# Kernel tuning notes

Measured on AMD Instinct MI355X. Metric: run time of the kernel, lower is better.

Reference implementation:

```python
import jax, jax.numpy as jnp
import numpy as np

# dims: n=batch, T=n_shifts, dX=16, dU=8, H=256 hidden, L=128 ldim, K=64 n_aux (L=2K)

def setup_inputs() -> dict:
    key = jax.random.key(0)
    ks = jax.random.split(key, 16)
    n, T, dX, dU, H, L, K = 64, 64, 16, 8, 256, 128, 64
    def lin(k, fan_in, shape):
        return (jax.random.uniform(k, shape, jnp.float32) * 2.0 - 1.0) / np.sqrt(fan_in)
    xs = jax.random.normal(ks[0], (n, T, dX), jnp.float32)
    us = jax.random.normal(ks[1], (n, T - 1, dU), jnp.float32)
    theta = jax.random.uniform(ks[2], (K,), jnp.float32) * (2.0 * np.pi)
    inp = {
        'xs': xs, 'us': us,
        # stacked x-aux encoders (K copies): BN affine, 3 linear layers (last no bias), output scale
        'x_gamma': jnp.ones((K, dX)), 'x_beta': jnp.zeros((K, dX)),
        'xW1': lin(ks[3], dX, (K, dX, H)), 'xb1': jnp.zeros((K, H)),
        'xW2': lin(ks[4], H, (K, H, H)), 'xb2': jnp.zeros((K, H)),
        'xW3': lin(ks[5], H, (K, H, L)), 'x_scale': jnp.ones((K, L)),
        # stacked u-aux encoders (K copies)
        'u_gamma': jnp.ones((K, dU)), 'u_beta': jnp.zeros((K, dU)),
        'uW1': lin(ks[6], dU, (K, dU, H)), 'ub1': jnp.zeros((K, H)),
        'uW2': lin(ks[7], H, (K, H, H)), 'ub2': jnp.zeros((K, H)),
        'uW3': lin(ks[8], H, (K, H, L)), 'u_scale': jnp.ones((K, L)),
        # Jordan-block complex eigenvalues (|lam| ~ 0.95)
        'reL': 0.95 * jnp.cos(theta), 'imL': 0.95 * jnp.sin(theta),
        # decoder C: Linear(ldim, dim, bias=False) -> weight [dX, L]
        'C_W': lin(ks[9], L, (dX, L)),
    }
    return inp


def _encoder(x, gamma, beta, W1, b1, W2, b2, W3, scale):
    # x: [M, D]; stacked params over K nets. BN stats (training mode) are per-feature over M,
    # identical across nets since the same x feeds every net.
    mu = x.mean(0)
    var = ((x - mu) ** 2).mean(0)
    xn = (x - mu) * jax.lax.rsqrt(var + 1e-5)          # [M, D]
    h = xn[None] * gamma[:, None, :] + beta[:, None, :]  # [K, M, D]
    h = jax.nn.leaky_relu(jnp.einsum('kmd,kdh->kmh', h, W1) + b1[:, None, :])
    h = jax.nn.leaky_relu(jnp.einsum('kmd,kdh->kmh', h, W2) + b2[:, None, :])
    h = jnp.einsum('kmd,kdh->kmh', h, W3)               # last layer: no bias
    return h * scale[:, None, :]                        # [K, M, L]


def reference(xs, us, x_gamma, x_beta, xW1, xb1, xW2, xb2, xW3, x_scale,
              u_gamma, u_beta, uW1, ub1, uW2, ub2, uW3, u_scale, reL, imL, C_W):
    n, T, dX = xs.shape
    K = reL.shape[0]
    L = 2 * K
    Tm1 = T - 1
    # phi1s: [n, T, K(net), K(pair), 2]
    phi = _encoder(xs.reshape(n * T, dX), x_gamma, x_beta, xW1, xb1, xW2, xb2, xW3, x_scale)
    phi1s = jnp.moveaxis(phi, 0, 1).reshape(n, T, K, K, 2)
    # ures = psi(u) - psi(0): [n, T-1, K, K, 2]
    uflat = us.reshape(n * Tm1, -1)
    psi_u = _encoder(uflat, u_gamma, u_beta, uW1, ub1, uW2, ub2, uW3, u_scale)
    psi_0 = _encoder(jnp.zeros_like(uflat), u_gamma, u_beta, uW1, ub1, uW2, ub2, uW3, u_scale)
    ures = jnp.moveaxis(psi_u - psi_0, 0, 1).reshape(n, Tm1, K, K, 2)
    # block-diagonal Koopman: per net j a 2x2 rotation-scale [[re, im], [-im, re]]
    R = jnp.stack([jnp.stack([reL, imL], -1), jnp.stack([-imL, reL], -1)], -2)  # [K, 2, 2]

    def step(p, u_t):
        p = jnp.einsum('bjkc,jcd->bjkd', p + u_t, R)
        return p, p

    _, preds = jax.lax.scan(step, phi1s[:, 0], jnp.moveaxis(ures, 0, 1))
    preds = jnp.moveaxis(preds, 0, 1)  # [n, T-1, K, K, 2]

    def phi2y(p):
        # sum over net axis (-3), flatten pair dims -> [.., L], decode with C
        return p.sum(-3).reshape(*p.shape[:-3], L) @ C_W.T

    y = phi2y(phi1s[:, 1:])
    y_pred = phi2y(preds)
    return y, y_pred
```

## Files before the change

kernel.cpp:

```cpp
#include <hip/hip_runtime.h>

typedef __bf16 bf16_t;
typedef __bf16 bf16x8 __attribute__((ext_vector_type(8)));
typedef __bf16 bf16x4 __attribute__((ext_vector_type(4)));
typedef float  f32x4  __attribute__((ext_vector_type(4)));

__global__ __launch_bounds__(256) void prep_all_kernel(
    const float* __restrict__ xW1, const float* __restrict__ xb1,
    const float* __restrict__ xg,  const float* __restrict__ xbeta,
    const float* __restrict__ uW1, const float* __restrict__ ub1,
    const float* __restrict__ ug,  const float* __restrict__ ubeta,
    const float* __restrict__ xW2, const float* __restrict__ uW2,
    const float* __restrict__ xW3, const float* __restrict__ uW3,
    const float* __restrict__ x_scale, const float* __restrict__ u_scale,
    const float* __restrict__ ub2,
    const float* __restrict__ xs, const float* __restrict__ us,
    bf16_t* __restrict__ xW1t, float* __restrict__ xb1p,
    bf16_t* __restrict__ uW1t, float* __restrict__ ub1p,
    bf16_t* __restrict__ xW2t, bf16_t* __restrict__ uW2t,
    bf16_t* __restrict__ xW3t, bf16_t* __restrict__ uW3t,
    float* __restrict__ psi0, float* __restrict__ part)
{
    const int t = blockIdx.x, tid = threadIdx.x;
    __shared__ float tile[32][33];
    __shared__ float h1[256], h2[256];

    if (t < 12288) {
        const float* in; bf16_t* outp; const float* scale = nullptr;
        int j, r0, c0, C;
        if (t < 8192) {
            C = 256;
            j = (t & 4095) >> 6;
            const int tl = t & 63; r0 = (tl >> 3) * 32; c0 = (tl & 7) * 32;
            if (t < 4096) { in = xW2; outp = xW2t; }
            else          { in = uW2; outp = uW2t; }
        } else {
            C = 128;
            const int l = t - 8192;
            j = (l & 2047) >> 5;
            const int tl = l & 31; r0 = (tl >> 2) * 32; c0 = (tl & 3) * 32;
            if (l < 2048) { in = xW3; outp = xW3t; scale = x_scale + j * 128; }
            else          { in = uW3; outp = uW3t; scale = u_scale + j * 128; }
        }
        const int R = 256;
        in   += (size_t)j * R * C;
        bf16_t* op = outp + (size_t)j * R * C;
        const int tx = tid & 31, ty = tid >> 5;
        #pragma unroll
        for (int i = 0; i < 4; i++)
            tile[ty + i * 8][tx] = in[(size_t)(r0 + ty + i * 8) * C + c0 + tx];
        __syncthreads();
        #pragma unroll
        for (int i = 0; i < 4; i++) {
            int c = c0 + ty + i * 8;
            float sc = scale ? scale[c] : 1.f;
            op[(size_t)c * R + r0 + tx] = (bf16_t)(tile[tx][ty + i * 8] * sc);
        }
    } else if (t < 12416) {
        const int bid = t - 12288, j = bid & 63, h = tid;
        const float *W1, *b1, *gamma, *beta; bf16_t* W1t; float* b1p; int D;
        if (bid < 64) { W1 = xW1; b1 = xb1; gamma = xg; beta = xbeta; W1t = xW1t; b1p = xb1p; D = 16; }
        else          { W1 = uW1; b1 = ub1; gamma = ug; beta = ubeta; W1t = uW1t; b1p = ub1p; D = 8; }
        float bacc = b1[j * 256 + h];
        bf16_t* orow = W1t + (size_t)(j * 256 + h) * 32;
        for (int d = 0; d < 32; d++) orow[d] = (bf16_t)0.f;
        for (int d = 0; d < D; d++) {
            float w = W1[((size_t)j * D + d) * 256 + h];
            orow[d] = (bf16_t)(gamma[j * D + d] * w);
            bacc += beta[j * D + d] * w;
        }
        b1p[j * 256 + h] = bacc;
    } else if (t < 12480) {
        const int j = t - 12416, h = tid;
        {
            float bacc = ub1[j * 256 + h];
            #pragma unroll
            for (int d = 0; d < 8; d++)
                bacc += ubeta[j * 8 + d] * uW1[((size_t)j * 8 + d) * 256 + h];
            h1[h] = fmaxf(bacc, 0.01f * bacc);
        }
        __syncthreads();
        {
            float acc = ub2[j * 256 + h];
            const float* w2 = uW2 + (size_t)j * 65536 + h;
            #pragma unroll 8
            for (int d = 0; d < 256; d++) acc += h1[d] * w2[d * 256];
            h2[h] = fmaxf(acc, 0.01f * acc);
        }
        __syncthreads();
        if (h < 128) {
            float acc = 0.f;
            const float* w3 = uW3 + (size_t)j * 32768 + h;
            #pragma unroll 8
            for (int d = 0; d < 256; d++) acc += h2[d] * w3[d * 128];
            psi0[j * 128 + h] = acc * u_scale[j * 128 + h];
        }
    } else {
        const int bid = t - 12480;
        const bool isx = bid < 64;
        const float* x = isx ? xs : us;
        const int D   = isx ? 16 : 8;
        const int lb  = isx ? bid : bid - 64;
        const int per = isx ? 1024 : 1008;
        const int start = lb * per;
        float a = 0.f, b = 0.f;
        for (int idx = start + tid; idx < start + per; idx += 256) {
            float v = x[idx];
            a += v; b += v * v;
        }
        float* s1 = h1; float* s2 = h2;
        s1[tid] = a; s2[tid] = b;
        __syncthreads();
        if (tid < D) {
            float sa = 0.f, sb = 0.f;
            for (int k = tid; k < 256; k += D) { sa += s1[k]; sb += s2[k]; }
            part[bid * 32 + tid]      = sa;
            part[bid * 32 + 16 + tid] = sb;
        }
    }
}

__global__ __launch_bounds__(512, 4) void fused_mlp_kernel(
    const float* __restrict__ xs, const float* __restrict__ us,
    const float* __restrict__ part,
    const bf16_t* __restrict__ xW1t, const float* __restrict__ xb1p,
    const bf16_t* __restrict__ xW2t, const float* __restrict__ xb2,
    const bf16_t* __restrict__ xW3t,
    const bf16_t* __restrict__ uW1t, const float* __restrict__ ub1p,
    const bf16_t* __restrict__ uW2t, const float* __restrict__ ub2,
    const bf16_t* __restrict__ uW3t,
    bf16_t* __restrict__ phi, bf16_t* __restrict__ psiu)
{
    const int bid  = blockIdx.x;
    const int xcd  = bid & 7;
    const int slot = bid >> 3;
    const int band = slot >> 6;
    const int t64  = slot & 63;
    const int j    = xcd * 8 + band;
    const bool is_x = t64 < 32;
    const int tile  = is_x ? t64 : (t64 - 32);

    const float*  In  = is_x ? xs   : us;
    const int     D   = is_x ? 16   : 8;
    const bf16_t* W1t = is_x ? xW1t : uW1t;
    const float*  b1p = is_x ? xb1p : ub1p;
    const bf16_t* W2t = is_x ? xW2t : uW2t;
    const float*  b2  = is_x ? xb2  : ub2;
    const bf16_t* W3t = is_x ? xW3t : uW3t;
    bf16_t* outp      = is_x ? phi  : psiu;
    const int M       = is_x ? 4096 : 4032;

    const int row0 = tile * 128;
    const int tid  = threadIdx.x;
    const int wave = tid >> 6;
    const int lane = tid & 63;
    const int quad = lane >> 4;
    const int l16  = lane & 15;
    const int lo2  = l16 & 3, hi2 = l16 >> 2;

    __shared__ __align__(16) bf16_t hs[128 * 256];
    __shared__ float stats_s[32];

    if (tid < 16) {
        if (is_x) {
            float sa = 0.f, sb = 0.f;
            #pragma unroll 8
            for (int b = 0; b < 64; b++) { sa += part[b * 32 + tid]; sb += part[b * 32 + 16 + tid]; }
            float mu = sa / 4096.f, var = sb / 4096.f - mu * mu;
            stats_s[tid] = mu; stats_s[16 + tid] = rsqrtf(var + 1e-5f);
        } else if (tid < 8) {
            float sa = 0.f, sb = 0.f;
            #pragma unroll 8
            for (int b = 64; b < 96; b++) { sa += part[b * 32 + tid]; sb += part[b * 32 + 16 + tid]; }
            float mu = sa / 4032.f, var = sb / 4032.f - mu * mu;
            stats_s[tid] = mu; stats_s[16 + tid] = rsqrtf(var + 1e-5f);
        }
    }
    __syncthreads();

    const f32x4 vzero = {0.f, 0.f, 0.f, 0.f};

    char* const hsB = (char*)hs;
    const char* const abase = hsB + l16 * 512 + ((quad ^ lo2) << 4);
    const int  wlow0 = (quad >> 1) ^ lo2;
    char* const wbase = hsB + l16 * 512 + ((wave ^ hi2) << 6) + ((quad & 1) << 3);

    {
        bf16x8 wfr[2];
        #pragma unroll
        for (int nbi = 0; nbi < 2; nbi++)
            wfr[nbi] = *reinterpret_cast<const bf16x8*>(
                W1t + (size_t)(j * 256 + wave * 32 + nbi * 16 + l16) * 32 + quad * 8);

        f32x4 acc[8][2];
        #pragma unroll
        for (int a = 0; a < 8; a++) { acc[a][0] = vzero; acc[a][1] = vzero; }

        const int c0 = quad * 8;
        #pragma unroll
        for (int mb = 0; mb < 8; mb++) {
            bf16x8 a;
            if (c0 < D) {
                int row = row0 + mb * 16 + l16;
                if (row > M - 1) row = M - 1;
                const float* xp = In + (size_t)row * D + c0;
                f32x4 v0 = *reinterpret_cast<const f32x4*>(xp);
                f32x4 v1 = *reinterpret_cast<const f32x4*>(xp + 4);
                #pragma unroll
                for (int e = 0; e < 4; e++) a[e]     = (bf16_t)((v0[e] - stats_s[c0 + e])     * stats_s[16 + c0 + e]);
                #pragma unroll
                for (int e = 0; e < 4; e++) a[4 + e] = (bf16_t)((v1[e] - stats_s[c0 + 4 + e]) * stats_s[16 + c0 + 4 + e]);
            } else {
                #pragma unroll
                for (int e = 0; e < 8; e++) a[e] = (bf16_t)0.f;
            }
            #pragma unroll
            for (int nbi = 0; nbi < 2; nbi++)
                acc[mb][nbi] = __builtin_amdgcn_mfma_f32_16x16x32_bf16(
                    wfr[nbi], a, acc[mb][nbi], 0, 0, 0);
        }

        #pragma unroll
        for (int nbi = 0; nbi < 2; nbi++) {
            const f32x4 bias = *reinterpret_cast<const f32x4*>(
                b1p + j * 256 + wave * 32 + nbi * 16 + quad * 4);
            char* wp = wbase + ((wlow0 ^ (nbi << 1)) << 4);
            #pragma unroll
            for (int mb = 0; mb < 8; mb++) {
                bf16x4 pk;
                #pragma unroll
                for (int r = 0; r < 4; r++) {
                    float v = acc[mb][nbi][r] + bias[r];
                    v = fmaxf(v, 0.01f * v);
                    pk[r] = (bf16_t)v;
                }
                *reinterpret_cast<bf16x4*>(wp + mb * 8192) = pk;
            }
        }
    }
    __syncthreads();

    {
        f32x4 acc[8][2];
        #pragma unroll
        for (int a = 0; a < 8; a++) { acc[a][0] = vzero; acc[a][1] = vzero; }

        const bf16_t* w2base = W2t + ((size_t)j * 256 + wave * 32 + l16) * 256 + quad * 8;

        bf16x8 wr[3][2];
        #pragma unroll
        for (int d = 0; d < 3; d++)
            #pragma unroll
            for (int nbi = 0; nbi < 2; nbi++)
                wr[d][nbi] = *reinterpret_cast<const bf16x8*>(w2base + nbi * 4096 + d * 32);

        #pragma unroll
        for (int kk = 0; kk < 8; kk++) {
            const int c = kk % 3;
            const char* ap = abase + ((kk ^ hi2) << 6);
            bf16x8 av0[4];
            #pragma unroll
            for (int mb = 0; mb < 4; mb++)
                av0[mb] = *reinterpret_cast<const bf16x8*>(ap + mb * 8192);
            #pragma unroll
            for (int nbi = 0; nbi < 2; nbi++)
                #pragma unroll
                for (int mb = 0; mb < 4; mb++)
                    acc[mb][nbi] = __builtin_amdgcn_mfma_f32_16x16x32_bf16(
                        wr[c][nbi], av0[mb], acc[mb][nbi], 0, 0, 0);
            bf16x8 av1[4];
            #pragma unroll
            for (int mb = 0; mb < 4; mb++)
                av1[mb] = *reinterpret_cast<const bf16x8*>(ap + (mb + 4) * 8192);
            #pragma unroll
            for (int nbi = 0; nbi < 2; nbi++)
                #pragma unroll
                for (int mb = 4; mb < 8; mb++)
                    acc[mb][nbi] = __builtin_amdgcn_mfma_f32_16x16x32_bf16(
                        wr[c][nbi], av1[mb - 4], acc[mb][nbi], 0, 0, 0);
            if (kk < 5) {
                #pragma unroll
                for (int nbi = 0; nbi < 2; nbi++)
                    wr[c][nbi] = *reinterpret_cast<const bf16x8*>(
                        w2base + nbi * 4096 + (kk + 3) * 32);
            }
        }
        __syncthreads();
        #pragma unroll
        for (int nbi = 0; nbi < 2; nbi++) {
            const f32x4 bias = *reinterpret_cast<const f32x4*>(
                b2 + j * 256 + wave * 32 + nbi * 16 + quad * 4);
            char* wp = wbase + ((wlow0 ^ (nbi << 1)) << 4);
            #pragma unroll
            for (int mb = 0; mb < 8; mb++) {
                bf16x4 pk;
                #pragma unroll
                for (int r = 0; r < 4; r++) {
                    float v = acc[mb][nbi][r] + bias[r];
                    v = fmaxf(v, 0.01f * v);
                    pk[r] = (bf16_t)v;
                }
                *reinterpret_cast<bf16x4*>(wp + mb * 8192) = pk;
            }
        }
    }
    __syncthreads();

    {
        f32x4 acc[8];
        #pragma unroll
        for (int a = 0; a < 8; a++) acc[a] = vzero;

        const bf16_t* w3base = W3t + ((size_t)j * 128 + wave * 16 + l16) * 256 + quad * 8;

        bf16x8 wr[3];
        #pragma unroll
        for (int d = 0; d < 3; d++)
            wr[d] = *reinterpret_cast<const bf16x8*>(w3base + d * 32);

        #pragma unroll
        for (int kk = 0; kk < 8; kk++) {
            const int c = kk % 3;
            const char* ap = abase + ((kk ^ hi2) << 6);
            bf16x8 av0[4];
            #pragma unroll
            for (int mb = 0; mb < 4; mb++)
                av0[mb] = *reinterpret_cast<const bf16x8*>(ap + mb * 8192);
            #pragma unroll
            for (int mb = 0; mb < 4; mb++)
                acc[mb] = __builtin_amdgcn_mfma_f32_16x16x32_bf16(
                    wr[c], av0[mb], acc[mb], 0, 0, 0);
            bf16x8 av1[4];
            #pragma unroll
            for (int mb = 0; mb < 4; mb++)
                av1[mb] = *reinterpret_cast<const bf16x8*>(ap + (mb + 4) * 8192);
            #pragma unroll
            for (int mb = 4; mb < 8; mb++)
                acc[mb] = __builtin_amdgcn_mfma_f32_16x16x32_bf16(
                    wr[c], av1[mb - 4], acc[mb], 0, 0, 0);
            if (kk < 5)
                wr[c] = *reinterpret_cast<const bf16x8*>(w3base + (kk + 3) * 32);
        }
        __syncthreads();
        {
            const int sp3 = (wave * 2 + (quad >> 1)) ^ l16;
            char* w3p = hsB + l16 * 256 + sp3 * 16 + ((quad & 1) << 3);
            #pragma unroll
            for (int mb = 0; mb < 8; mb++) {
                bf16x4 pk;
                #pragma unroll
                for (int r = 0; r < 4; r++) pk[r] = (bf16_t)acc[mb][r];
                *reinterpret_cast<bf16x4*>(w3p + mb * 4096) = pk;
            }
        }
    }
    __syncthreads();
    #pragma unroll
    for (int p = 0; p < 4; p++) {
        const int rr = p * 32 + (tid >> 4);
        const int s  = tid & 15;
        if (row0 + rr < M) {
            bf16x8 v = *reinterpret_cast<const bf16x8*>(hs + rr * 128 + (s ^ (rr & 15)) * 8);
            *reinterpret_cast<bf16x8*>(outp + ((size_t)j * M + row0 + rr) * 128 + s * 8) = v;
        }
    }
}

__global__ __launch_bounds__(256) void y_kernel(
    const bf16_t* __restrict__ phi, const float* __restrict__ C_W,
    float* __restrict__ y) {
    const int m0 = blockIdx.x * 16;
    const int tid = threadIdx.x;
    __shared__ float S[16][128];
    __shared__ float Cs[2048];
    #pragma unroll
    for (int i = 0; i < 8; i++) Cs[tid + i * 256] = C_W[tid + i * 256];
    const int r  = tid >> 4;
    const int cg = (tid & 15) * 8;
    float acc[8];
    #pragma unroll
    for (int e = 0; e < 8; e++) acc[e] = 0.f;
    const bf16_t* p = phi + (size_t)(m0 + r) * 128 + cg;
    for (int j = 0; j < 64; j++) {
        bf16x8 v = *reinterpret_cast<const bf16x8*>(p + (size_t)j * 524288);
        #pragma unroll
        for (int e = 0; e < 8; e++) acc[e] += (float)v[e];
    }
    #pragma unroll
    for (int e = 0; e < 8; e++) S[r][cg + e] = acc[e];
    __syncthreads();
    const int mm = tid >> 4, o = tid & 15;
    const int m = m0 + mm;
    if ((m & 63) != 0) {
        float a = 0.f;
        #pragma unroll 8
        for (int l = 0; l < 128; l++) a += S[mm][l] * Cs[o * 128 + l];
        const int b = m >> 6, ti = (m & 63) - 1;
        y[(b * 63 + ti) * 16 + o] = a;
    }
}

__global__ __launch_bounds__(256) void scan_kernel(
    const bf16_t* __restrict__ phi, const bf16_t* __restrict__ psiu,
    const float* __restrict__ psi0, const float* __restrict__ reL,
    const float* __restrict__ imL, float* __restrict__ scratch) {
    const int b = blockIdx.x >> 3, jg = blockIdx.x & 7;
    const int tid = threadIdx.x;
    const int wave = tid >> 6, lane = tid & 63;
    __shared__ float red[2][4][128];

    const int j0 = jg * 8 + wave * 2;
    float sx0, sy0, sx1, sy1;
    float p0x0, p0y0, p0x1, p0y1, lre0, lim0, lre1, lim1;
    {
        unsigned v0 = *reinterpret_cast<const unsigned*>(
            phi + ((size_t)j0 * 4096 + b * 64) * 128 + lane * 2);
        unsigned v1 = *reinterpret_cast<const unsigned*>(
            phi + ((size_t)(j0 + 1) * 4096 + b * 64) * 128 + lane * 2);
        sx0 = __uint_as_float(v0 << 16); sy0 = __uint_as_float(v0 & 0xFFFF0000u);
        sx1 = __uint_as_float(v1 << 16); sy1 = __uint_as_float(v1 & 0xFFFF0000u);
        float2 p0 = *reinterpret_cast<const float2*>(psi0 + j0 * 128 + lane * 2);
        float2 p1 = *reinterpret_cast<const float2*>(psi0 + (j0 + 1) * 128 + lane * 2);
        p0x0 = p0.x; p0y0 = p0.y; p0x1 = p1.x; p0y1 = p1.y;
        lre0 = reL[j0]; lim0 = imL[j0]; lre1 = reL[j0 + 1]; lim1 = imL[j0 + 1];
    }
    const bf16_t* up0 = psiu + ((size_t)j0 * 4032 + b * 63) * 128 + lane * 2;
    const bf16_t* up1 = psiu + ((size_t)(j0 + 1) * 4032 + b * 63) * 128 + lane * 2;
    unsigned cur0 = *reinterpret_cast<const unsigned*>(up0);
    unsigned cur1 = *reinterpret_cast<const unsigned*>(up1);
    float* out = scratch + (size_t)blockIdx.x * 63 * 128;

    for (int t = 0; t < 63; t++) {
        unsigned nx0 = 0, nx1 = 0;
        if (t < 62) {
            nx0 = *reinterpret_cast<const unsigned*>(up0 + (t + 1) * 128);
            nx1 = *reinterpret_cast<const unsigned*>(up1 + (t + 1) * 128);
        }
        float px = sx0 + (__uint_as_float(cur0 << 16) - p0x0);
        float py = sy0 + (__uint_as_float(cur0 & 0xFFFF0000u) - p0y0);
        sx0 = px * lre0 - py * lim0;
        sy0 = px * lim0 + py * lre0;
        px = sx1 + (__uint_as_float(cur1 << 16) - p0x1);
        py = sy1 + (__uint_as_float(cur1 & 0xFFFF0000u) - p0y1);
        sx1 = px * lre1 - py * lim1;
        sy1 = px * lim1 + py * lre1;
        const int db = t & 1;
        red[db][wave][lane * 2]     = sx0 + sx1;
        red[db][wave][lane * 2 + 1] = sy0 + sy1;
        __syncthreads();
        if (tid < 128)
            out[t * 128 + tid] = red[db][0][tid] + red[db][1][tid]
                               + red[db][2][tid] + red[db][3][tid];
        cur0 = nx0; cur1 = nx1;
    }
}

__global__ __launch_bounds__(64) void decode_kernel(
    const float* __restrict__ scratch, const float* __restrict__ C_W,
    float* __restrict__ ypred) {
    const int t = blockIdx.x, b = blockIdx.y, l = threadIdx.x;
    __shared__ float S[128];
    float s0 = 0.f, s1 = 0.f;
    #pragma unroll
    for (int jg = 0; jg < 8; jg++) {
        float2 v = *reinterpret_cast<const float2*>(
            scratch + ((size_t)(b * 8 + jg) * 63 + t) * 128 + l * 2);
        s0 += v.x; s1 += v.y;
    }
    S[l * 2] = s0; S[l * 2 + 1] = s1;
    __syncthreads();
    const int o = l >> 2, q = l & 3;
    float acc = 0.f;
    #pragma unroll
    for (int i = 0; i < 32; i++)
        acc += S[q * 32 + i] * C_W[o * 128 + q * 32 + i];
    acc += __shfl_xor(acc, 2, 4);
    acc += __shfl_xor(acc, 1, 4);
    if (q == 0) ypred[(b * 63 + t) * 16 + o] = acc;
}

extern "C" void kernel_launch(void* const* d_in, const int* in_sizes, int n_in,
                              void* d_out, int out_size, void* d_ws, size_t ws_size,
                              hipStream_t stream) {
    const float* xs      = (const float*)d_in[0];
    const float* us      = (const float*)d_in[1];
    const float* x_gamma = (const float*)d_in[2];
    const float* x_beta  = (const float*)d_in[3];
    const float* xW1     = (const float*)d_in[4];
    const float* xb1     = (const float*)d_in[5];
    const float* xW2     = (const float*)d_in[6];
    const float* xb2     = (const float*)d_in[7];
    const float* xW3     = (const float*)d_in[8];
    const float* x_scale = (const float*)d_in[9];
    const float* u_gamma = (const float*)d_in[10];
    const float* u_beta  = (const float*)d_in[11];
    const float* uW1     = (const float*)d_in[12];
    const float* ub1     = (const float*)d_in[13];
    const float* uW2     = (const float*)d_in[14];
    const float* ub2     = (const float*)d_in[15];
    const float* uW3     = (const float*)d_in[16];
    const float* u_scale = (const float*)d_in[17];
    const float* reL     = (const float*)d_in[18];
    const float* imL     = (const float*)d_in[19];
    const float* C_W     = (const float*)d_in[20];

    char* ws = (char*)d_ws;
    size_t off = 0;
    auto alloc = [&](size_t bytes) -> char* {
        char* p = ws + off;
        off += (bytes + 255) & ~(size_t)255;
        return p;
    };
    float*  part = (float*)alloc(96 * 32 * 4);
    bf16_t* xW1t = (bf16_t*)alloc((size_t)64 * 256 * 32 * 2);
    float*  xb1p = (float*) alloc((size_t)64 * 256 * 4);
    bf16_t* xW2t = (bf16_t*)alloc((size_t)64 * 256 * 256 * 2);
    bf16_t* xW3t = (bf16_t*)alloc((size_t)64 * 128 * 256 * 2);
    bf16_t* uW1t = (bf16_t*)alloc((size_t)64 * 256 * 32 * 2);
    float*  ub1p = (float*) alloc((size_t)64 * 256 * 4);
    bf16_t* uW2t = (bf16_t*)alloc((size_t)64 * 256 * 256 * 2);
    bf16_t* uW3t = (bf16_t*)alloc((size_t)64 * 128 * 256 * 2);
    float*  psi0 = (float*) alloc((size_t)64 * 128 * 4);
    bf16_t* phi  = (bf16_t*)alloc((size_t)64 * 4096 * 128 * 2);
    bf16_t* psiu = (bf16_t*)alloc((size_t)64 * 4032 * 128 * 2);
    float*  scr  = (float*) alloc((size_t)512 * 63 * 128 * 4);

    float* y_out     = (float*)d_out;
    float* ypred_out = y_out + 64 * 63 * 16;

    prep_all_kernel<<<12576, 256, 0, stream>>>(
        xW1, xb1, x_gamma, x_beta, uW1, ub1, u_gamma, u_beta,
        xW2, uW2, xW3, uW3, x_scale, u_scale, ub2, xs, us,
        xW1t, xb1p, uW1t, ub1p, xW2t, uW2t, xW3t, uW3t, psi0, part);
    fused_mlp_kernel<<<4096, 512, 0, stream>>>(
        xs, us, part,
        xW1t, xb1p, xW2t, xb2, xW3t, uW1t, ub1p, uW2t, ub2, uW3t, phi, psiu);
    y_kernel<<<256, 256, 0, stream>>>(phi, C_W, y_out);
    scan_kernel<<<512, 256, 0, stream>>>(phi, psiu, psi0, reL, imL, scr);
    decode_kernel<<<dim3(63, 64), 64, 0, stream>>>(scr, C_W, ypred_out);
}
```

Before: 362.7 us.

## Retile fused MLP waves to 64x64 output blocks and merge y and scan kernels

The fused MLP now splits its 8 waves into a 2x4 grid, so each wave computes a 64-row by 64-column tile instead of all 128 rows by 32 columns. This halves the LDS activation reads per MFMA and reuses each A fragment across four weight fragments. The shared-memory write swizzle and the layer-2 weight prefetch (now double-buffered) are rewritten to match. Separately, the y-decode and scan kernels are merged into one launch, with block index choosing the role, to save a kernel launch and let both run concurrently.

```diff
diff --git a/kernel.cpp b/kernel.cpp
--- a/kernel.cpp
+++ b/kernel.cpp
@@ -158,6 +158,12 @@
     const int l16  = lane & 15;
     const int lo2  = l16 & 3, hi2 = l16 >> 2;
 
+    const int nw = wave & 3;
+    const int mw = wave >> 2;
+    const int m0 = mw * 64;
+    const int n0 = nw * 64;
+    const int n3 = (wave & 3) * 32;
+
     __shared__ __align__(16) bf16_t hs[128 * 256];
     __shared__ float stats_s[32];
 
@@ -181,27 +187,27 @@
     const f32x4 vzero = {0.f, 0.f, 0.f, 0.f};
 
     char* const hsB = (char*)hs;
-    const char* const abase = hsB + l16 * 512 + ((quad ^ lo2) << 4);
-    const int  wlow0 = (quad >> 1) ^ lo2;
-    char* const wbase = hsB + l16 * 512 + ((wave ^ hi2) << 6) + ((quad & 1) << 3);
+    const char* const abase = hsB + (m0 + l16) * 512 + ((quad ^ lo2) << 4);
 
     {
-        bf16x8 wfr[2];
-        #pragma unroll
-        for (int nbi = 0; nbi < 2; nbi++)
+        bf16x8 wfr[4];
+        #pragma unroll
+        for (int nbi = 0; nbi < 4; nbi++)
             wfr[nbi] = *reinterpret_cast<const bf16x8*>(
-                W1t + (size_t)(j * 256 + wave * 32 + nbi * 16 + l16) * 32 + quad * 8);
-
-        f32x4 acc[8][2];
-        #pragma unroll
-        for (int a = 0; a < 8; a++) { acc[a][0] = vzero; acc[a][1] = vzero; }
+                W1t + (size_t)(j * 256 + n0 + nbi * 16 + l16) * 32 + quad * 8);
+
+        f32x4 acc[4][4];
+        #pragma unroll
+        for (int a = 0; a < 4; a++)
+            #pragma unroll
+            for (int c = 0; c < 4; c++) acc[a][c] = vzero;
 
         const int c0 = quad * 8;
         #pragma unroll
-        for (int mb = 0; mb < 8; mb++) {
+        for (int mb = 0; mb < 4; mb++) {
             bf16x8 a;
             if (c0 < D) {
-                int row = row0 + mb * 16 + l16;
+                int row = row0 + m0 + mb * 16 + l16;
                 if (row > M - 1) row = M - 1;
                 const float* xp = In + (size_t)row * D + c0;
                 f32x4 v0 = *reinterpret_cast<const f32x4*>(xp);
@@ -215,18 +221,19 @@
                 for (int e = 0; e < 8; e++) a[e] = (bf16_t)0.f;
             }
             #pragma unroll
-            for (int nbi = 0; nbi < 2; nbi++)
+            for (int nbi = 0; nbi < 4; nbi++)
                 acc[mb][nbi] = __builtin_amdgcn_mfma_f32_16x16x32_bf16(
                     wfr[nbi], a, acc[mb][nbi], 0, 0, 0);
         }
 
         #pragma unroll
-        for (int nbi = 0; nbi < 2; nbi++) {
+        for (int nbi = 0; nbi < 4; nbi++) {
             const f32x4 bias = *reinterpret_cast<const f32x4*>(
-                b1p + j * 256 + wave * 32 + nbi * 16 + quad * 4);
-            char* wp = wbase + ((wlow0 ^ (nbi << 1)) << 4);
-            #pragma unroll
-            for (int mb = 0; mb < 8; mb++) {
+                b1p + j * 256 + n0 + nbi * 16 + quad * 4);
+            const int g = (n0 >> 3) + nbi * 2 + (quad >> 1);
+            char* wrow = hsB + (m0 + l16) * 512 + ((g ^ l16) << 4) + ((quad & 1) << 3);
+            #pragma unroll
+            for (int mb = 0; mb < 4; mb++) {
                 bf16x4 pk;
                 #pragma unroll
                 for (int r = 0; r < 4; r++) {
@@ -234,65 +241,56 @@
                     v = fmaxf(v, 0.01f * v);
                     pk[r] = (bf16_t)v;
                 }
-                *reinterpret_cast<bf16x4*>(wp + mb * 8192) = pk;
+                *reinterpret_cast<bf16x4*>(wrow + mb * 8192) = pk;
             }
         }
     }
     __syncthreads();
 
     {
-        f32x4 acc[8][2];
-        #pragma unroll
-        for (int a = 0; a < 8; a++) { acc[a][0] = vzero; acc[a][1] = vzero; }
-
-        const bf16_t* w2base = W2t + ((size_t)j * 256 + wave * 32 + l16) * 256 + quad * 8;
-
-        bf16x8 wr[3][2];
-        #pragma unroll
-        for (int d = 0; d < 3; d++)
-            #pragma unroll
-            for (int nbi = 0; nbi < 2; nbi++)
-                wr[d][nbi] = *reinterpret_cast<const bf16x8*>(w2base + nbi * 4096 + d * 32);
+        f32x4 acc[4][4];
+        #pragma unroll
+        for (int a = 0; a < 4; a++)
+            #pragma unroll
+            for (int c = 0; c < 4; c++) acc[a][c] = vzero;
+
+        const bf16_t* w2base = W2t + ((size_t)j * 256 + n0 + l16) * 256 + quad * 8;
+
+        bf16x8 wr[2][4];
+        #pragma unroll
+        for (int nbi = 0; nbi < 4; nbi++)
+            wr[0][nbi] = *reinterpret_cast<const bf16x8*>(w2base + nbi * 4096);
 
         #pragma unroll
         for (int kk = 0; kk < 8; kk++) {
-            const int c = kk % 3;
+            const int cb = kk & 1, nb = cb ^ 1;
+            if (kk < 7) {
+                #pragma unroll
+                for (int nbi = 0; nbi < 4; nbi++)
+                    wr[nb][nbi] = *reinterpret_cast<const bf16x8*>(
+                        w2base + nbi * 4096 + (kk + 1) * 32);
+            }
             const char* ap = abase + ((kk ^ hi2) << 6);
-            bf16x8 av0[4];
+            bf16x8 av[4];
             #pragma unroll
             for (int mb = 0; mb < 4; mb++)
-                av0[mb] = *reinterpret_cast<const bf16x8*>(ap + mb * 8192);
-            #pragma unroll
-            for (int nbi = 0; nbi < 2; nbi++)
+                av[mb] = *reinterpret_cast<const bf16x8*>(ap + mb * 8192);
+            #pragma unroll
+            for (int nbi = 0; nbi < 4; nbi++)
                 #pragma unroll
                 for (int mb = 0; mb < 4; mb++)
                     acc[mb][nbi] = __builtin_amdgcn_mfma_f32_16x16x32_bf16(
-                        wr[c][nbi], av0[mb], acc[mb][nbi], 0, 0, 0);
-            bf16x8 av1[4];
-            #pragma unroll
-            for (int mb = 0; mb < 4; mb++)
-                av1[mb] = *reinterpret_cast<const bf16x8*>(ap + (mb + 4) * 8192);
-            #pragma unroll
-            for (int nbi = 0; nbi < 2; nbi++)
-                #pragma unroll
-                for (int mb = 4; mb < 8; mb++)
-                    acc[mb][nbi] = __builtin_amdgcn_mfma_f32_16x16x32_bf16(
-                        wr[c][nbi], av1[mb - 4], acc[mb][nbi], 0, 0, 0);
-            if (kk < 5) {
-                #pragma unroll
-                for (int nbi = 0; nbi < 2; nbi++)
-                    wr[c][nbi] = *reinterpret_cast<const bf16x8*>(
-                        w2base + nbi * 4096 + (kk + 3) * 32);
-            }
-        }
-        __syncthreads();
-        #pragma unroll
-        for (int nbi = 0; nbi < 2; nbi++) {
+                        wr[cb][nbi], av[mb], acc[mb][nbi], 0, 0, 0);
+        }
+        __syncthreads();
+        #pragma unroll
+        for (int nbi = 0; nbi < 4; nbi++) {
             const f32x4 bias = *reinterpret_cast<const f32x4*>(
-                b2 + j * 256 + wave * 32 + nbi * 16 + quad * 4);
-            char* wp = wbase + ((wlow0 ^ (nbi << 1)) << 4);
-            #pragma unroll
-            for (int mb = 0; mb < 8; mb++) {
+                b2 + j * 256 + n0 + nbi * 16 + quad * 4);
+            const int g = (n0 >> 3) + nbi * 2 + (quad >> 1);
+            char* wrow = hsB + (m0 + l16) * 512 + ((g ^ l16) << 4) + ((quad & 1) << 3);
+            #pragma unroll
+            for (int mb = 0; mb < 4; mb++) {
                 bf16x4 pk;
                 #pragma unroll
                 for (int r = 0; r < 4; r++) {
@@ -300,57 +298,58 @@
                     v = fmaxf(v, 0.01f * v);
                     pk[r] = (bf16_t)v;
                 }
-                *reinterpret_cast<bf16x4*>(wp + mb * 8192) = pk;
+                *reinterpret_cast<bf16x4*>(wrow + mb * 8192) = pk;
             }
         }
     }
     __syncthreads();
 
     {
-        f32x4 acc[8];
-        #pragma unroll
-        for (int a = 0; a < 8; a++) acc[a] = vzero;
-
-        const bf16_t* w3base = W3t + ((size_t)j * 128 + wave * 16 + l16) * 256 + quad * 8;
-
-        bf16x8 wr[3];
+        f32x4 acc[4][2];
+        #pragma unroll
+        for (int a = 0; a < 4; a++) { acc[a][0] = vzero; acc[a][1] = vzero; }
+
+        const bf16_t* w3base = W3t + ((size_t)j * 128 + n3 + l16) * 256 + quad * 8;
+
+        bf16x8 wr[3][2];
         #pragma unroll
         for (int d = 0; d < 3; d++)
-            wr[d] = *reinterpret_cast<const bf16x8*>(w3base + d * 32);
+            #pragma unroll
+            for (int nbi = 0; nbi < 2; nbi++)
+                wr[d][nbi] = *reinterpret_cast<const bf16x8*>(w3base + nbi * 4096 + d * 32);
 
         #pragma unroll
         for (int kk = 0; kk < 8; kk++) {
             const int c = kk % 3;
             const char* ap = abase + ((kk ^ hi2) << 6);
-            bf16x8 av0[4];
+            bf16x8 av[4];
             #pragma unroll
             for (int mb = 0; mb < 4; mb++)
-                av0[mb] = *reinterpret_cast<const bf16x8*>(ap + mb * 8192);
-            #pragma unroll
-            for (int mb = 0; mb < 4; mb++)
-                acc[mb] = __builtin_amdgcn_mfma_f32_16x16x32_bf16(
-                    wr[c], av0[mb], acc[mb], 0, 0, 0);
-            bf16x8 av1[4];
-            #pragma unroll
-            for (int mb = 0; mb < 4; mb++)
-                av1[mb] = *reinterpret_cast<const bf16x8*>(ap + (mb + 4) * 8192);
-            #pragma unroll
-            for (int mb = 4; mb < 8; mb++)
-                acc[mb] = __builtin_amdgcn_mfma_f32_16x16x32_bf16(
-                    wr[c], av1[mb - 4], acc[mb], 0, 0, 0);
-            if (kk < 5)
-                wr[c] = *reinterpret_cast<const bf16x8*>(w3base + (kk + 3) * 32);
-        }
-        __syncthreads();
-        {
-            const int sp3 = (wave * 2 + (quad >> 1)) ^ l16;
-            char* w3p = hsB + l16 * 256 + sp3 * 16 + ((quad & 1) << 3);
-            #pragma unroll
-            for (int mb = 0; mb < 8; mb++) {
+                av[mb] = *reinterpret_cast<const bf16x8*>(ap + mb * 8192);
+            #pragma unroll
+            for (int nbi = 0; nbi < 2; nbi++)
+                #pragma unroll
+                for (int mb = 0; mb < 4; mb++)
+                    acc[mb][nbi] = __builtin_amdgcn_mfma_f32_16x16x32_bf16(
+                        wr[c][nbi], av[mb], acc[mb][nbi], 0, 0, 0);
+            if (kk < 5) {
+                #pragma unroll
+                for (int nbi = 0; nbi < 2; nbi++)
+                    wr[c][nbi] = *reinterpret_cast<const bf16x8*>(
+                        w3base + nbi * 4096 + (kk + 3) * 32);
+            }
+        }
+        __syncthreads();
+        #pragma unroll
+        for (int nbi = 0; nbi < 2; nbi++) {
+            const int g = (n3 >> 3) + nbi * 2 + (quad >> 1);
+            char* wrow = hsB + (m0 + l16) * 256 + ((g ^ l16) << 4) + ((quad & 1) << 3);
+            #pragma unroll
+            for (int mb = 0; mb < 4; mb++) {
                 bf16x4 pk;
                 #pragma unroll
-                for (int r = 0; r < 4; r++) pk[r] = (bf16_t)acc[mb][r];
-                *reinterpret_cast<bf16x4*>(w3p + mb * 4096) = pk;
+                for (int r = 0; r < 4; r++) pk[r] = (bf16_t)acc[mb][nbi][r];
+                *reinterpret_cast<bf16x4*>(wrow + mb * 4096) = pk;
             }
         }
     }
@@ -366,48 +365,48 @@
     }
 }
 
-__global__ __launch_bounds__(256) void y_kernel(
-    const bf16_t* __restrict__ phi, const float* __restrict__ C_W,
-    float* __restrict__ y) {
-    const int m0 = blockIdx.x * 16;
+__global__ __launch_bounds__(256) void scan_y_kernel(
+    const bf16_t* __restrict__ phi, const bf16_t* __restrict__ psiu,
+    const float* __restrict__ psi0, const float* __restrict__ reL,
+    const float* __restrict__ imL, const float* __restrict__ C_W,
+    float* __restrict__ scratch, float* __restrict__ y) {
     const int tid = threadIdx.x;
+    __shared__ float red[2][4][128];
     __shared__ float S[16][128];
     __shared__ float Cs[2048];
-    #pragma unroll
-    for (int i = 0; i < 8; i++) Cs[tid + i * 256] = C_W[tid + i * 256];
-    const int r  = tid >> 4;
-    const int cg = (tid & 15) * 8;
-    float acc[8];
-    #pragma unroll
-    for (int e = 0; e < 8; e++) acc[e] = 0.f;
-    const bf16_t* p = phi + (size_t)(m0 + r) * 128 + cg;
-    for (int j = 0; j < 64; j++) {
-        bf16x8 v = *reinterpret_cast<const bf16x8*>(p + (size_t)j * 524288);
-        #pragma unroll
-        for (int e = 0; e < 8; e++) acc[e] += (float)v[e];
-    }
-    #pragma unroll
-    for (int e = 0; e < 8; e++) S[r][cg + e] = acc[e];
-    __syncthreads();
-    const int mm = tid >> 4, o = tid & 15;
-    const int m = m0 + mm;
-    if ((m & 63) != 0) {
-        float a = 0.f;
-        #pragma unroll 8
-        for (int l = 0; l < 128; l++) a += S[mm][l] * Cs[o * 128 + l];
-        const int b = m >> 6, ti = (m & 63) - 1;
-        y[(b * 63 + ti) * 16 + o] = a;
-    }
-}
-
-__global__ __launch_bounds__(256) void scan_kernel(
-    const bf16_t* __restrict__ phi, const bf16_t* __restrict__ psiu,
-    const float* __restrict__ psi0, const float* __restrict__ reL,
-    const float* __restrict__ imL, float* __restrict__ scratch) {
+
+    if (blockIdx.x >= 512) {
+        const int m0 = (blockIdx.x - 512) * 16;
+        #pragma unroll
+        for (int i = 0; i < 8; i++) Cs[tid + i * 256] = C_W[tid + i * 256];
+        const int r  = tid >> 4;
+        const int cg = (tid & 15) * 8;
+        float acc[8];
+        #pragma unroll
+        for (int e = 0; e < 8; e++) acc[e] = 0.f;
+        const bf16_t* p = phi + (size_t)(m0 + r) * 128 + cg;
+        for (int j = 0; j < 64; j++) {
+            bf16x8 v = *reinterpret_cast<const bf16x8*>(p + (size_t)j * 524288);
+            #pragma unroll
+            for (int e = 0; e < 8; e++) acc[e] += (float)v[e];
+        }
+        #pragma unroll
+        for (int e = 0; e < 8; e++) S[r][cg + e] = acc[e];
+        __syncthreads();
+        const int mm = tid >> 4, o = tid & 15;
+        const int m = m0 + mm;
+        if ((m & 63) != 0) {
+            float a = 0.f;
+            #pragma unroll 8
+            for (int l = 0; l < 128; l++) a += S[mm][l] * Cs[o * 128 + l];
+            const int b = m >> 6, ti = (m & 63) - 1;
+            y[(b * 63 + ti) * 16 + o] = a;
+        }
+        return;
+    }
+
     const int b = blockIdx.x >> 3, jg = blockIdx.x & 7;
-    const int tid = threadIdx.x;
     const int wave = tid >> 6, lane = tid & 63;
-    __shared__ float red[2][4][128];
 
     const int j0 = jg * 8 + wave * 2;
     float sx0, sy0, sx1, sy1;
@@ -535,7 +534,6 @@
     fused_mlp_kernel<<<4096, 512, 0, stream>>>(
         xs, us, part,
         xW1t, xb1p, xW2t, xb2, xW3t, uW1t, ub1p, uW2t, ub2, uW3t, phi, psiu);
-    y_kernel<<<256, 256, 0, stream>>>(phi, C_W, y_out);
-    scan_kernel<<<512, 256, 0, stream>>>(phi, psiu, psi0, reL, imL, scr);
+    scan_y_kernel<<<768, 256, 0, stream>>>(phi, psiu, psi0, reL, imL, C_W, scr, y_out);
     decode_kernel<<<dim3(63, 64), 64, 0, stream>>>(scr, C_W, ypred_out);
 }
```

New measurement: 433.3 us. 1.19x slower.

## Fuse y, scan and decode kernels; enlarge transpose tiles in prep

Applied to the files above, without the earlier changes.

Merges y_kernel, scan_kernel and decode_kernel into one 512-thread kernel. Blocks 0-63 each run the full per-batch scan over all 64 nets and decode y_pred in place, so the fp32 scratch buffer and its round trip go away. Blocks 64 and up compute y with 4-way unrolled loads. The weight-transpose part of prep now uses 64x32 tiles, which halves its block count. The trade-off is less scan parallelism (64 blocks instead of 512) and an extra barrier per timestep, in exchange for two fewer launches and less global traffic.

```diff
diff --git a/kernel.cpp b/kernel.cpp
--- a/kernel.cpp
+++ b/kernel.cpp
@@ -22,42 +22,42 @@
     float* __restrict__ psi0, float* __restrict__ part)
 {
     const int t = blockIdx.x, tid = threadIdx.x;
-    __shared__ float tile[32][33];
+    __shared__ float tile[32][65];
     __shared__ float h1[256], h2[256];
 
-    if (t < 12288) {
+    if (t < 6144) {
         const float* in; bf16_t* outp; const float* scale = nullptr;
         int j, r0, c0, C;
-        if (t < 8192) {
+        if (t < 4096) {
             C = 256;
-            j = (t & 4095) >> 6;
-            const int tl = t & 63; r0 = (tl >> 3) * 32; c0 = (tl & 7) * 32;
-            if (t < 4096) { in = xW2; outp = xW2t; }
+            j = (t & 2047) >> 5;
+            const int tl = t & 31; r0 = (tl >> 3) * 64; c0 = (tl & 7) * 32;
+            if (t < 2048) { in = xW2; outp = xW2t; }
             else          { in = uW2; outp = uW2t; }
         } else {
             C = 128;
-            const int l = t - 8192;
-            j = (l & 2047) >> 5;
-            const int tl = l & 31; r0 = (tl >> 2) * 32; c0 = (tl & 3) * 32;
-            if (l < 2048) { in = xW3; outp = xW3t; scale = x_scale + j * 128; }
+            const int l = t - 4096;
+            j = (l & 1023) >> 4;
+            const int tl = l & 15; r0 = (tl >> 2) * 64; c0 = (tl & 3) * 32;
+            if (l < 1024) { in = xW3; outp = xW3t; scale = x_scale + j * 128; }
             else          { in = uW3; outp = uW3t; scale = u_scale + j * 128; }
         }
-        const int R = 256;
-        in   += (size_t)j * R * C;
-        bf16_t* op = outp + (size_t)j * R * C;
-        const int tx = tid & 31, ty = tid >> 5;
-        #pragma unroll
-        for (int i = 0; i < 4; i++)
-            tile[ty + i * 8][tx] = in[(size_t)(r0 + ty + i * 8) * C + c0 + tx];
-        __syncthreads();
-        #pragma unroll
-        for (int i = 0; i < 4; i++) {
-            int c = c0 + ty + i * 8;
-            float sc = scale ? scale[c] : 1.f;
-            op[(size_t)c * R + r0 + tx] = (bf16_t)(tile[tx][ty + i * 8] * sc);
-        }
-    } else if (t < 12416) {
-        const int bid = t - 12288, j = bid & 63, h = tid;
+        in += (size_t)j * 256 * C;
+        bf16_t* op = outp + (size_t)j * 256 * C;
+        const int cx = tid & 31, ry0 = tid >> 5;
+        #pragma unroll
+        for (int p = 0; p < 8; p++)
+            tile[cx][ry0 + p * 8] = in[(size_t)(r0 + ry0 + p * 8) * C + c0 + cx];
+        __syncthreads();
+        const int rr = tid & 63, cb = tid >> 6;
+        #pragma unroll
+        for (int p = 0; p < 8; p++) {
+            const int cl = cb + p * 4;
+            float sc = scale ? scale[c0 + cl] : 1.f;
+            op[(size_t)(c0 + cl) * 256 + r0 + rr] = (bf16_t)(tile[cl][rr] * sc);
+        }
+    } else if (t < 6272) {
+        const int bid = t - 6144, j = bid & 63, h = tid;
         const float *W1, *b1, *gamma, *beta; bf16_t* W1t; float* b1p; int D;
         if (bid < 64) { W1 = xW1; b1 = xb1; gamma = xg; beta = xbeta; W1t = xW1t; b1p = xb1p; D = 16; }
         else          { W1 = uW1; b1 = ub1; gamma = ug; beta = ubeta; W1t = uW1t; b1p = ub1p; D = 8; }
@@ -70,8 +70,8 @@
             bacc += beta[j * D + d] * w;
         }
         b1p[j * 256 + h] = bacc;
-    } else if (t < 12480) {
-        const int j = t - 12416, h = tid;
+    } else if (t < 6336) {
+        const int j = t - 6272, h = tid;
         {
             float bacc = ub1[j * 256 + h];
             #pragma unroll
@@ -96,7 +96,7 @@
             psi0[j * 128 + h] = acc * u_scale[j * 128 + h];
         }
     } else {
-        const int bid = t - 12480;
+        const int bid = t - 6336;
         const bool isx = bid < 64;
         const float* x = isx ? xs : us;
         const int D   = isx ? 16 : 8;
@@ -366,117 +366,117 @@
     }
 }
 
-__global__ __launch_bounds__(256) void y_kernel(
-    const bf16_t* __restrict__ phi, const float* __restrict__ C_W,
-    float* __restrict__ y) {
-    const int m0 = blockIdx.x * 16;
-    const int tid = threadIdx.x;
-    __shared__ float S[16][128];
-    __shared__ float Cs[2048];
-    #pragma unroll
-    for (int i = 0; i < 8; i++) Cs[tid + i * 256] = C_W[tid + i * 256];
-    const int r  = tid >> 4;
-    const int cg = (tid & 15) * 8;
-    float acc[8];
-    #pragma unroll
-    for (int e = 0; e < 8; e++) acc[e] = 0.f;
-    const bf16_t* p = phi + (size_t)(m0 + r) * 128 + cg;
-    for (int j = 0; j < 64; j++) {
-        bf16x8 v = *reinterpret_cast<const bf16x8*>(p + (size_t)j * 524288);
-        #pragma unroll
-        for (int e = 0; e < 8; e++) acc[e] += (float)v[e];
-    }
-    #pragma unroll
-    for (int e = 0; e < 8; e++) S[r][cg + e] = acc[e];
-    __syncthreads();
-    const int mm = tid >> 4, o = tid & 15;
-    const int m = m0 + mm;
-    if ((m & 63) != 0) {
-        float a = 0.f;
-        #pragma unroll 8
-        for (int l = 0; l < 128; l++) a += S[mm][l] * Cs[o * 128 + l];
-        const int b = m >> 6, ti = (m & 63) - 1;
-        y[(b * 63 + ti) * 16 + o] = a;
-    }
-}
-
-__global__ __launch_bounds__(256) void scan_kernel(
+__global__ __launch_bounds__(512) void scan_y_kernel(
     const bf16_t* __restrict__ phi, const bf16_t* __restrict__ psiu,
     const float* __restrict__ psi0, const float* __restrict__ reL,
-    const float* __restrict__ imL, float* __restrict__ scratch) {
-    const int b = blockIdx.x >> 3, jg = blockIdx.x & 7;
+    const float* __restrict__ imL, const float* __restrict__ C_W,
+    float* __restrict__ y, float* __restrict__ ypred) {
     const int tid = threadIdx.x;
+    __shared__ float Cs[2048];
+    __shared__ float red[2][8][128];
+    __shared__ float S2[2][128];
+    __shared__ float S[32][128];
+
+    #pragma unroll
+    for (int i = 0; i < 4; i++) Cs[tid + i * 512] = C_W[tid + i * 512];
+
+    if (blockIdx.x >= 64) {
+        const int m0 = (blockIdx.x - 64) * 32;
+        const int r  = tid >> 4;
+        const int cg = (tid & 15) * 8;
+        float acc[8];
+        #pragma unroll
+        for (int e = 0; e < 8; e++) acc[e] = 0.f;
+        const bf16_t* p = phi + (size_t)(m0 + r) * 128 + cg;
+        for (int j = 0; j < 64; j += 4) {
+            bf16x8 v0 = *reinterpret_cast<const bf16x8*>(p + (size_t)j * 524288);
+            bf16x8 v1 = *reinterpret_cast<const bf16x8*>(p + (size_t)(j + 1) * 524288);
+            bf16x8 v2 = *reinterpret_cast<const bf16x8*>(p + (size_t)(j + 2) * 524288);
+            bf16x8 v3 = *reinterpret_cast<const bf16x8*>(p + (size_t)(j + 3) * 524288);
+            #pragma unroll
+            for (int e = 0; e < 8; e++)
+                acc[e] += (float)v0[e] + (float)v1[e] + (float)v2[e] + (float)v3[e];
+        }
+        #pragma unroll
+        for (int e = 0; e < 8; e++) S[r][cg + e] = acc[e];
+        __syncthreads();
+        const int mm = tid >> 4, o = tid & 15;
+        const int m = m0 + mm;
+        if ((m & 63) != 0) {
+            float a = 0.f;
+            #pragma unroll 8
+            for (int l = 0; l < 128; l++) a += S[mm][l] * Cs[o * 128 + l];
+            const int b = m >> 6, ti = (m & 63) - 1;
+            y[(b * 63 + ti) * 16 + o] = a;
+        }
+        return;
+    }
+
+    const int b = blockIdx.x;
     const int wave = tid >> 6, lane = tid & 63;
-    __shared__ float red[2][4][128];
-
-    const int j0 = jg * 8 + wave * 2;
-    float sx0, sy0, sx1, sy1;
-    float p0x0, p0y0, p0x1, p0y1, lre0, lim0, lre1, lim1;
-    {
-        unsigned v0 = *reinterpret_cast<const unsigned*>(
-            phi + ((size_t)j0 * 4096 + b * 64) * 128 + lane * 2);
-        unsigned v1 = *reinterpret_cast<const unsigned*>(
-            phi + ((size_t)(j0 + 1) * 4096 + b * 64) * 128 + lane * 2);
-        sx0 = __uint_as_float(v0 << 16); sy0 = __uint_as_float(v0 & 0xFFFF0000u);
-        sx1 = __uint_as_float(v1 << 16); sy1 = __uint_as_float(v1 & 0xFFFF0000u);
-        float2 p0 = *reinterpret_cast<const float2*>(psi0 + j0 * 128 + lane * 2);
-        float2 p1 = *reinterpret_cast<const float2*>(psi0 + (j0 + 1) * 128 + lane * 2);
-        p0x0 = p0.x; p0y0 = p0.y; p0x1 = p1.x; p0y1 = p1.y;
-        lre0 = reL[j0]; lim0 = imL[j0]; lre1 = reL[j0 + 1]; lim1 = imL[j0 + 1];
-    }
-    const bf16_t* up0 = psiu + ((size_t)j0 * 4032 + b * 63) * 128 + lane * 2;
-    const bf16_t* up1 = psiu + ((size_t)(j0 + 1) * 4032 + b * 63) * 128 + lane * 2;
-    unsigned cur0 = *reinterpret_cast<const unsigned*>(up0);
-    unsigned cur1 = *reinterpret_cast<const unsigned*>(up1);
-    float* out = scratch + (size_t)blockIdx.x * 63 * 128;
+    const int j0 = wave * 8;
+
+    float sx[8], sy[8], p0x[8], p0y[8], lre[8], lim[8];
+    #pragma unroll
+    for (int i = 0; i < 8; i++) {
+        const int j = j0 + i;
+        unsigned v = *reinterpret_cast<const unsigned*>(
+            phi + ((size_t)j * 4096 + b * 64) * 128 + lane * 2);
+        sx[i] = __uint_as_float(v << 16);
+        sy[i] = __uint_as_float(v & 0xFFFF0000u);
+        float2 p0 = *reinterpret_cast<const float2*>(psi0 + j * 128 + lane * 2);
+        p0x[i] = p0.x; p0y[i] = p0.y;
+        lre[i] = reL[j]; lim[i] = imL[j];
+    }
+    const bf16_t* upb = psiu + ((size_t)j0 * 4032 + b * 63) * 128 + lane * 2;
+    unsigned cur[8];
+    #pragma unroll
+    for (int i = 0; i < 8; i++)
+        cur[i] = *reinterpret_cast<const unsigned*>(upb + (size_t)i * 516096);
+    __syncthreads();
 
     for (int t = 0; t < 63; t++) {
-        unsigned nx0 = 0, nx1 = 0;
+        unsigned nxt[8];
         if (t < 62) {
-            nx0 = *reinterpret_cast<const unsigned*>(up0 + (t + 1) * 128);
-            nx1 = *reinterpret_cast<const unsigned*>(up1 + (t + 1) * 128);
-        }
-        float px = sx0 + (__uint_as_float(cur0 << 16) - p0x0);
-        float py = sy0 + (__uint_as_float(cur0 & 0xFFFF0000u) - p0y0);
-        sx0 = px * lre0 - py * lim0;
-        sy0 = px * lim0 + py * lre0;
-        px = sx1 + (__uint_as_float(cur1 << 16) - p0x1);
-        py = sy1 + (__uint_as_float(cur1 & 0xFFFF0000u) - p0y1);
-        sx1 = px * lre1 - py * lim1;
-        sy1 = px * lim1 + py * lre1;
+            #pragma unroll
+            for (int i = 0; i < 8; i++)
+                nxt[i] = *reinterpret_cast<const unsigned*>(
+                    upb + (size_t)i * 516096 + (t + 1) * 128);
+        }
+        float lsx = 0.f, lsy = 0.f;
+        #pragma unroll
+        for (int i = 0; i < 8; i++) {
+            float px = sx[i] + (__uint_as_float(cur[i] << 16) - p0x[i]);
+            float py = sy[i] + (__uint_as_float(cur[i] & 0xFFFF0000u) - p0y[i]);
+            sx[i] = px * lre[i] - py * lim[i];
+            sy[i] = px * lim[i] + py * lre[i];
+            lsx += sx[i]; lsy += sy[i];
+        }
         const int db = t & 1;
-        red[db][wave][lane * 2]     = sx0 + sx1;
-        red[db][wave][lane * 2 + 1] = sy0 + sy1;
-        __syncthreads();
-        if (tid < 128)
-            out[t * 128 + tid] = red[db][0][tid] + red[db][1][tid]
-                               + red[db][2][tid] + red[db][3][tid];
-        cur0 = nx0; cur1 = nx1;
-    }
-}
-
-__global__ __launch_bounds__(64) void decode_kernel(
-    const float* __restrict__ scratch, const float* __restrict__ C_W,
-    float* __restrict__ ypred) {
-    const int t = blockIdx.x, b = blockIdx.y, l = threadIdx.x;
-    __shared__ float S[128];
-    float s0 = 0.f, s1 = 0.f;
-    #pragma unroll
-    for (int jg = 0; jg < 8; jg++) {
-        float2 v = *reinterpret_cast<const float2*>(
-            scratch + ((size_t)(b * 8 + jg) * 63 + t) * 128 + l * 2);
-        s0 += v.x; s1 += v.y;
-    }
-    S[l * 2] = s0; S[l * 2 + 1] = s1;
-    __syncthreads();
-    const int o = l >> 2, q = l & 3;
-    float acc = 0.f;
-    #pragma unroll
-    for (int i = 0; i < 32; i++)
-        acc += S[q * 32 + i] * C_W[o * 128 + q * 32 + i];
-    acc += __shfl_xor(acc, 2, 4);
-    acc += __shfl_xor(acc, 1, 4);
-    if (q == 0) ypred[(b * 63 + t) * 16 + o] = acc;
+        red[db][wave][lane * 2]     = lsx;
+        red[db][wave][lane * 2 + 1] = lsy;
+        __syncthreads();
+        if (tid < 128) {
+            float s = 0.f;
+            #pragma unroll
+            for (int w = 0; w < 8; w++) s += red[db][w][tid];
+            S2[db][tid] = s;
+        }
+        __syncthreads();
+        if (tid < 128) {
+            const int o = tid >> 3, sub = tid & 7;
+            float a = 0.f;
+            #pragma unroll
+            for (int i = 0; i < 16; i++)
+                a += S2[db][sub * 16 + i] * Cs[o * 128 + sub * 16 + i];
+            a += __shfl_xor(a, 4);
+            a += __shfl_xor(a, 2);
+            a += __shfl_xor(a, 1);
+            if (sub == 0) ypred[(b * 63 + t) * 16 + o] = a;
+        }
+        #pragma unroll
+        for (int i = 0; i < 8; i++) cur[i] = nxt[i];
+    }
 }
 
 extern "C" void kernel_launch(void* const* d_in, const int* in_sizes, int n_in,
@@ -523,19 +523,17 @@
     float*  psi0 = (float*) alloc((size_t)64 * 128 * 4);
     bf16_t* phi  = (bf16_t*)alloc((size_t)64 * 4096 * 128 * 2);
     bf16_t* psiu = (bf16_t*)alloc((size_t)64 * 4032 * 128 * 2);
-    float*  scr  = (float*) alloc((size_t)512 * 63 * 128 * 4);
 
     float* y_out     = (float*)d_out;
     float* ypred_out = y_out + 64 * 63 * 16;
 
-    prep_all_kernel<<<12576, 256, 0, stream>>>(
+    prep_all_kernel<<<6432, 256, 0, stream>>>(
         xW1, xb1, x_gamma, x_beta, uW1, ub1, u_gamma, u_beta,
         xW2, uW2, xW3, uW3, x_scale, u_scale, ub2, xs, us,
         xW1t, xb1p, uW1t, ub1p, xW2t, uW2t, xW3t, uW3t, psi0, part);
     fused_mlp_kernel<<<4096, 512, 0, stream>>>(
         xs, us, part,
         xW1t, xb1p, xW2t, xb2, xW3t, uW1t, ub1p, uW2t, ub2, uW3t, phi, psiu);
-    y_kernel<<<256, 256, 0, stream>>>(phi, C_W, y_out);
-    scan_kernel<<<512, 256, 0, stream>>>(phi, psiu, psi0, reL, imL, scr);
-    decode_kernel<<<dim3(63, 64), 64, 0, stream>>>(scr, C_W, ypred_out);
+    scan_y_kernel<<<192, 512, 0, stream>>>(
+        phi, psiu, psi0, reL, imL, C_W, y_out, ypred_out);
 }
```

New measurement: 368.1 us. No clear change (+1.5%).
